# Kernel optimization log

Hardware: AMD Instinct MI355X
Metric: run time of the kernel (lower is better)

Reference implementation:

```python
import jax, jax.numpy as jnp
import numpy as np

B, DIM, L = 4, 1024, 4096
N_CODES, CODE_DIM, H = 512, 256, 8
D = DIM // H  # head_dim = 128


def setup_inputs() -> dict:
    key = jax.random.key(0)
    k1, k2, k3, k4 = jax.random.split(key, 4)
    return {
        "x": jax.random.normal(k1, (B, DIM, L), dtype=jnp.float32),
        "codes": jax.random.normal(k2, (N_CODES, CODE_DIM), dtype=jnp.float32),
        "Wk": jax.random.normal(k3, (CODE_DIM, H, D), dtype=jnp.float32) * (CODE_DIM ** -0.5),
        "Wv": jax.random.normal(k4, (CODE_DIM, H, D), dtype=jnp.float32) * (CODE_DIM ** -0.5),
    }


def reference(x, codes, Wk, Wv):
    b, xdim, l = x.shape
    h, d = Wk.shape[1], Wk.shape[2]
    scale = d ** -0.5
    # b (h d) l -> b h l d
    q = scale * jnp.transpose(x.reshape(b, h, d, l), (0, 1, 3, 2))
    k = jnp.einsum('nc,chd->hnd', codes, Wk)  # [H, N, D]
    v = jnp.einsum('nc,chd->hnd', codes, Wv)  # [H, N, D]
    logits = jnp.einsum('bhld,hmd->bhlm', q, k)  # [B, H, L, N]
    idx = jnp.argmax(logits, axis=-1)  # [B, H, L] int
    # hard one-hot attention == direct gather from v
    h_ix = jnp.arange(h)[None, :, None]  # broadcast over B, L
    out = v[h_ix, idx]  # [B, H, L, D]
    out = jnp.transpose(out, (0, 1, 3, 2)).reshape(b, h * d, l)  # b (h d) l
    return out, idx
```

## Files before the change

kernel.cpp:

```cpp
#include <hip/hip_runtime.h>
#include <cstdint>

#define L_ 4096
#define NC_ 512
#define CD_ 256
#define H_ 8
#define D_ 128
#define B_ 4
#define SCALE 0.08838834764831845f
#define TAU 3.0e-3f

typedef _Float16 f16x8 __attribute__((ext_vector_type(8)));
typedef _Float16 f16x4 __attribute__((ext_vector_type(4)));
typedef float f32x16 __attribute__((ext_vector_type(16)));
typedef float f32x4 __attribute__((ext_vector_type(4)));

__global__ __launch_bounds__(256) void kv_pre(
    const float* __restrict__ codes, const float* __restrict__ Wk,
    const float* __restrict__ Wv, _Float16* __restrict__ K16f,
    float* __restrict__ K32, float* __restrict__ V)
{
    __shared__ float clds[16][260];
    const int t = threadIdx.x, h = blockIdx.y, n0 = blockIdx.x * 16;
    const int dz = blockIdx.z;
    {
        #pragma unroll
        for (int i = 0; i < 4; ++i) {
            int j = t + i*256;
            int row = j >> 6, c4 = j & 63;
            *(float4*)&clds[row][c4*4] =
                *(const float4*)(codes + (size_t)(n0 + row)*CD_ + c4*4);
        }
    }
    __syncthreads();
    const int nl = t >> 4;
    const int dq = t & 15;
    const int d0 = dz*64 + dq*4;
    const int n  = n0 + nl;
    float ak0=0,ak1=0,ak2=0,ak3=0, av0=0,av1=0,av2=0,av3=0;
    const float4* wk4 = (const float4*)Wk;
    const float4* wv4 = (const float4*)Wv;
    for (int c = 0; c < CD_; c += 4) {
        float4 cv = *(const float4*)&clds[nl][c];
        #pragma unroll
        for (int u = 0; u < 4; ++u) {
            float cu = (u==0)?cv.x:(u==1)?cv.y:(u==2)?cv.z:cv.w;
            float4 wk = wk4[((size_t)(c+u)*H_ + h)*32 + (d0>>2)];
            float4 wv = wv4[((size_t)(c+u)*H_ + h)*32 + (d0>>2)];
            ak0 = fmaf(cu, wk.x, ak0); ak1 = fmaf(cu, wk.y, ak1);
            ak2 = fmaf(cu, wk.z, ak2); ak3 = fmaf(cu, wk.w, ak3);
            av0 = fmaf(cu, wv.x, av0); av1 = fmaf(cu, wv.y, av1);
            av2 = fmaf(cu, wv.z, av2); av3 = fmaf(cu, wv.w, av3);
        }
    }
    const size_t r32 = ((size_t)(h*NC_ + n))*D_ + d0;
    float4 sk; sk.x=ak0; sk.y=ak1; sk.z=ak2; sk.w=ak3;
    float4 sv; sv.x=av0; sv.y=av1; sv.z=av2; sv.w=av3;
    *(float4*)(K32 + r32) = sk;
    *(float4*)(V   + r32) = sv;
    f16x4 hk; hk[0]=(_Float16)ak0; hk[1]=(_Float16)ak1; hk[2]=(_Float16)ak2; hk[3]=(_Float16)ak3;
    const size_t a16 = ((size_t)((h*16 + (n>>5))*8 + (d0>>4))*64
                        + ((n&31) + ((d0>>3)&1)*32))*8 + (d0&7);
    *(f16x4*)(K16f + a16) = hk;
}

#define GLD_LDS16(GP, LP)                                                      \
  __builtin_amdgcn_global_load_lds(                                            \
      (const __attribute__((address_space(1))) void*)(GP),                     \
      (__attribute__((address_space(3))) void*)(LP), 16, 0, 0)

#define WAIT_VM0    asm volatile("s_waitcnt vmcnt(0)" ::: "memory")
#define WAIT_LGKM   asm volatile("s_waitcnt lgkmcnt(0)" ::: "memory")

#define QSTAGE(RD, QS)                                                         \
  _Pragma("unroll")                                                            \
  for (int i_ = 0; i_ < 4; ++i_) {                                             \
    const float* sp_ = xb + (size_t)((RD)*32 + i_*8 + (lane>>3))*L_            \
                          + l0w + (lane&7)*4;                                  \
    GLD_LDS16(sp_, (char*)(QS) + i_*1024);                                     \
  }

#define QREAD(RD, QS)                                                          \
  _Pragma("unroll")                                                            \
  for (int p_ = 0; p_ < 2; ++p_) {                                             \
    f16x8 tmp_;                                                                \
    _Pragma("unroll")                                                          \
    for (int j_ = 0; j_ < 8; ++j_)                                             \
      tmp_[j_] = (_Float16)(SCALE * (QS)[(p_*16 + hi*8 + j_)*32 + colL]);      \
    qf[(RD)*2 + p_] = tmp_;                                                    \
  }

#define KSTAGE(TI, DST)                                                        \
  GLD_LDS16(kh + ((size_t)(TI)*4096 + (wid*64 + lane)*8),                      \
            (DST) + (size_t)(wid*64)*8);                                       \
  GLD_LDS16(kh + ((size_t)(TI)*4096 + (256 + wid*64 + lane)*8),                \
            (DST) + (size_t)(256 + wid*64)*8);

__global__ __launch_bounds__(256, 4) void attn_main(
    const float* __restrict__ x, const _Float16* __restrict__ K16f,
    const float* __restrict__ K32, const float* __restrict__ V,
    float* __restrict__ out, float* __restrict__ idxf)
{
    __shared__ __align__(16) char smem[32768 + 2048];
    _Float16* bufA = (_Float16*)smem;
    _Float16* bufB = (_Float16*)(smem + 16384);
    float*    qbuf = (float*)(smem + 32768);

    const int t = threadIdx.x;
    const int wid = t >> 6, lane = t & 63;
    const int bid = blockIdx.x;
    const int h  = bid & 7;
    const int rr_ = bid >> 3;
    const int lx = rr_ & 31, b = rr_ >> 5;
    const int l0w = lx * 128 + wid * 32;

    const float* xb = x + ((size_t)(b*1024 + h*128)) * L_;
    const int colL = lane & 31;
    const int hi = lane >> 5;
    const int laneN4 = hi * 4;

    float* qs0 = (float*)(smem + wid * 8192);
    float* qs1 = (float*)(smem + wid * 8192 + 4096);
    f16x8 qf[8];
    QSTAGE(0, qs0)
    QSTAGE(1, qs1)
    WAIT_VM0;
    QREAD(0, qs0)
    QREAD(1, qs1)
    WAIT_LGKM;
    QSTAGE(2, qs0)
    QSTAGE(3, qs1)
    WAIT_VM0;
    QREAD(2, qs0)
    QREAD(3, qs1)
    __syncthreads();

    const _Float16* kh = K16f + ((size_t)h << 16);

    KSTAGE(0, bufA)
    KSTAGE(1, bufA + 4096)

    float v1 = -INFINITY, v2 = -INFINITY, v3 = -INFINITY;
    int i1 = 0, i2 = 0;

    __syncthreads();

    for (int m = 0; m < 8; ++m) {
        _Float16* cur = (m & 1) ? bufB : bufA;
        _Float16* nxt = (m & 1) ? bufA : bufB;
        if (m < 7) {
            KSTAGE(2*m + 2, nxt)
            KSTAGE(2*m + 3, nxt + 4096)
        }
        #pragma unroll
        for (int sub = 0; sub < 2; ++sub) {
            const _Float16* kt = cur + sub*4096;
            f32x16 acc;
            #pragma unroll
            for (int r = 0; r < 16; ++r) acc[r] = 0.f;
            #pragma unroll
            for (int ds = 0; ds < 8; ++ds) {
                f16x8 kf = *(const f16x8*)(kt + (size_t)(ds*64 + lane)*8);
                acc = __builtin_amdgcn_mfma_f32_32x32x16_f16(kf, qf[ds], acc, 0, 0, 0);
            }
            const int nb = (2*m + sub)*32 + laneN4;
            #pragma unroll
            for (int r = 0; r < 16; ++r) {
                const int n = nb + (r & 3) + ((r >> 2) << 3);
                float v = acc[r];
                bool gt1 = v > v1;
                bool gt2 = v > v2;
                i2 = gt1 ? i1 : (gt2 ? n : i2);
                i1 = gt1 ? n  : i1;
                v3 = fmaxf(v3, fminf(v2, v));
                v2 = fmaxf(v2, fminf(v1, v));
                v1 = fmaxf(v1, v);
            }
        }
        __syncthreads();
    }

    float ov1 = __shfl_xor(v1, 32), ov2 = __shfl_xor(v2, 32), ov3 = __shfl_xor(v3, 32);
    int oi1 = __shfl_xor(i1, 32), oi2 = __shfl_xor(i2, 32);
    bool sw = (ov1 > v1) || (ov1 == v1 && oi1 < i1);
    float a1 = sw ? ov1 : v1;  int ai1 = sw ? oi1 : i1;
    float b1 = sw ? v1 : ov1;  int bi1 = sw ? i1 : oi1;
    float a2 = sw ? ov2 : v2;  int ai2 = sw ? oi2 : i2;
    float b2 = sw ? v2 : ov2;
    float a3 = sw ? ov3 : v3;
    bool sec = (b1 > a2) || (b1 == a2 && bi1 < ai2);
    const float V1 = a1;             const int I1 = ai1;
    const float V2 = sec ? b1 : a2;  const int I2 = sec ? bi1 : ai2;
    const float V3 = sec ? fmaxf(a2, b2) : fmaxf(a3, b1);
    int idx = I1;

    const bool cheap = (V1 - V2 < TAU) && (V1 - V3 >= TAU);
    const bool full  = (V1 - V3 < TAU);

    unsigned long long mc = __ballot(cheap) & 0xffffffffull;
    while (mc) {
        int src = (int)__builtin_ctzll(mc); mc &= mc - 1;
        int rl = l0w + src;
        int ra = __shfl(I1, src);
        int rb = __shfl(I2, src);
        int n = hi ? rb : ra;
        f32x4 kk = *(const f32x4*)(K32 + ((size_t)(h*NC_ + n))*D_ + colL*4);
        int dd = colL * 4;
        float q0 = SCALE * xb[(size_t)(dd+0)*L_ + rl];
        float q1 = SCALE * xb[(size_t)(dd+1)*L_ + rl];
        float q2 = SCALE * xb[(size_t)(dd+2)*L_ + rl];
        float q3 = SCALE * xb[(size_t)(dd+3)*L_ + rl];
        float p = q0 * kk[0];
        p = fmaf(q1, kk[1], p); p = fmaf(q2, kk[2], p); p = fmaf(q3, kk[3], p);
        #pragma unroll
        for (int m2 = 1; m2 < 32; m2 <<= 1) p += __shfl_xor(p, m2);
        float va = __shfl(p, 0);
        float vb = __shfl(p, 32);
        bool takeB = (vb > va) || (vb == va && rb < ra);
        int win = takeB ? rb : ra;
        if (lane == src) idx = win;
    }

    unsigned long long mf2 = __ballot(full) & 0xffffffffull;
    float* qb = qbuf + wid * 128;
    while (mf2) {
        int src = (int)__builtin_ctzll(mf2); mf2 &= mf2 - 1;
        int rl = l0w + src;
        qb[lane]      = SCALE * xb[(size_t)lane*L_ + rl];
        qb[lane + 64] = SCALE * xb[(size_t)(lane+64)*L_ + rl];
        __builtin_amdgcn_wave_barrier();
        WAIT_LGKM;
        float q0 = qb[colL*4+0], q1 = qb[colL*4+1], q2 = qb[colL*4+2], q3 = qb[colL*4+3];
        const f32x4* krow = (const f32x4*)(K32 + (size_t)h*NC_*D_);
        float bv = -INFINITY; int bn = 0;
        for (int i = 0; i < 256; i += 4) {
            #pragma unroll
            for (int u = 0; u < 4; ++u) {
                f32x4 kk = krow[(size_t)(i+u)*64 + lane];
                float p = q0 * kk[0];
                p = fmaf(q1, kk[1], p); p = fmaf(q2, kk[2], p); p = fmaf(q3, kk[3], p);
                #pragma unroll
                for (int m2 = 1; m2 < 32; m2 <<= 1) p += __shfl_xor(p, m2);
                const int n = 2*(i+u) + hi;
                if (p > bv) { bv = p; bn = n; }
            }
        }
        {
            float ov = __shfl_xor(bv, 32);
            int on = __shfl_xor(bn, 32);
            if (ov > bv || (ov == bv && on < bn)) { bv = ov; bn = on; }
        }
        if (lane == src) idx = bn;
        __builtin_amdgcn_wave_barrier();
    }
    idx = __shfl(idx, colL);

    const int myl = l0w + colL;
    if (!hi) idxf[((size_t)(b*H_ + h))*L_ + myl] = (float)idx;
    const f32x4* vrow = (const f32x4*)(V + ((size_t)(h*NC_ + idx))*D_);
    float* ob = out + ((size_t)(b*1024 + h*128 + hi*64))*L_ + myl;
    #pragma unroll
    for (int p = 0; p < 16; ++p) {
        f32x4 vv = vrow[hi*16 + p];
        ob[(size_t)(p*4+0)*L_] = vv[0];
        ob[(size_t)(p*4+1)*L_] = vv[1];
        ob[(size_t)(p*4+2)*L_] = vv[2];
        ob[(size_t)(p*4+3)*L_] = vv[3];
    }
}

extern "C" void kernel_launch(void* const* d_in, const int* in_sizes, int n_in,
                              void* d_out, int out_size, void* d_ws, size_t ws_size,
                              hipStream_t stream)
{
    const float* x     = (const float*)d_in[0];
    const float* codes = (const float*)d_in[1];
    const float* Wk    = (const float*)d_in[2];
    const float* Wv    = (const float*)d_in[3];

    float* out  = (float*)d_out;
    float* idxf = out + (size_t)B_ * H_ * D_ * L_;

    _Float16* K16f = (_Float16*)d_ws;
    float*    K32  = (float*)((char*)d_ws + (1u << 20));
    float*    Vf   = (float*)((char*)d_ws + (3u << 20));

    kv_pre<<<dim3(32, 8, 2), 256, 0, stream>>>(codes, Wk, Wv, K16f, K32, Vf);
    attn_main<<<dim3(1024), 256, 0, stream>>>(x, K16f, K32, Vf, out, idxf);
}
```

Baseline: 104.4 us.

## Pack code index into float low bits for branchless top-3 argmax tracking

```diff
diff --git a/kernel.cpp b/kernel.cpp
--- a/kernel.cpp
+++ b/kernel.cpp
@@ -8,7 +8,7 @@
 #define D_ 128
 #define B_ 4
 #define SCALE 0.08838834764831845f
-#define TAU 3.0e-3f
+#define TAU 4.0e-3f
 
 typedef _Float16 f16x8 __attribute__((ext_vector_type(8)));
 typedef _Float16 f16x4 __attribute__((ext_vector_type(4)));
@@ -58,7 +58,9 @@
     float4 sv; sv.x=av0; sv.y=av1; sv.z=av2; sv.w=av3;
     *(float4*)(K32 + r32) = sk;
     *(float4*)(V   + r32) = sv;
-    f16x4 hk; hk[0]=(_Float16)ak0; hk[1]=(_Float16)ak1; hk[2]=(_Float16)ak2; hk[3]=(_Float16)ak3;
+    f16x4 hk;
+    hk[0]=(_Float16)(SCALE*ak0); hk[1]=(_Float16)(SCALE*ak1);
+    hk[2]=(_Float16)(SCALE*ak2); hk[3]=(_Float16)(SCALE*ak3);
     const size_t a16 = ((size_t)((h*16 + (n>>5))*8 + (d0>>4))*64
                         + ((n&31) + ((d0>>3)&1)*32))*8 + (d0&7);
     *(f16x4*)(K16f + a16) = hk;
@@ -86,7 +88,7 @@
     f16x8 tmp_;                                                                \
     _Pragma("unroll")                                                          \
     for (int j_ = 0; j_ < 8; ++j_)                                             \
-      tmp_[j_] = (_Float16)(SCALE * (QS)[(p_*16 + hi*8 + j_)*32 + colL]);      \
+      tmp_[j_] = (_Float16)((QS)[(p_*16 + hi*8 + j_)*32 + colL]);              \
     qf[(RD)*2 + p_] = tmp_;                                                    \
   }
 
@@ -140,8 +142,10 @@
     KSTAGE(0, bufA)
     KSTAGE(1, bufA + 4096)
 
+    int nOr[16];
+    #pragma unroll
+    for (int r = 0; r < 16; ++r) nOr[r] = (r & 3) + ((r >> 2) << 3) + laneN4;
     float v1 = -INFINITY, v2 = -INFINITY, v3 = -INFINITY;
-    int i1 = 0, i2 = 0;
 
     __syncthreads();
 
@@ -163,35 +167,30 @@
                 f16x8 kf = *(const f16x8*)(kt + (size_t)(ds*64 + lane)*8);
                 acc = __builtin_amdgcn_mfma_f32_32x32x16_f16(kf, qf[ds], acc, 0, 0, 0);
             }
-            const int nb = (2*m + sub)*32 + laneN4;
+            const int tb = (2*m + sub)*32;
             #pragma unroll
             for (int r = 0; r < 16; ++r) {
-                const int n = nb + (r & 3) + ((r >> 2) << 3);
-                float v = acc[r];
-                bool gt1 = v > v1;
-                bool gt2 = v > v2;
-                i2 = gt1 ? i1 : (gt2 ? n : i2);
-                i1 = gt1 ? n  : i1;
-                v3 = fmaxf(v3, fminf(v2, v));
-                v2 = fmaxf(v2, fminf(v1, v));
-                v1 = fmaxf(v1, v);
+                int ki = (__float_as_int(acc[r]) & 0xFFFFFE00) | (tb + nOr[r]);
+                float k = __int_as_float(ki);
+                v3 = fmaxf(v3, fminf(fminf(v1, v2), k));
+                float nv2 = __builtin_amdgcn_fmed3f(v1, v2, k);
+                v1 = fmaxf(v1, k);
+                v2 = nv2;
             }
         }
         __syncthreads();
     }
 
-    float ov1 = __shfl_xor(v1, 32), ov2 = __shfl_xor(v2, 32), ov3 = __shfl_xor(v3, 32);
-    int oi1 = __shfl_xor(i1, 32), oi2 = __shfl_xor(i2, 32);
-    bool sw = (ov1 > v1) || (ov1 == v1 && oi1 < i1);
-    float a1 = sw ? ov1 : v1;  int ai1 = sw ? oi1 : i1;
-    float b1 = sw ? v1 : ov1;  int bi1 = sw ? i1 : oi1;
-    float a2 = sw ? ov2 : v2;  int ai2 = sw ? oi2 : i2;
-    float b2 = sw ? v2 : ov2;
-    float a3 = sw ? ov3 : v3;
-    bool sec = (b1 > a2) || (b1 == a2 && bi1 < ai2);
-    const float V1 = a1;             const int I1 = ai1;
-    const float V2 = sec ? b1 : a2;  const int I2 = sec ? bi1 : ai2;
-    const float V3 = sec ? fmaxf(a2, b2) : fmaxf(a3, b1);
+    float b1k = __shfl_xor(v1, 32);
+    float b2k = __shfl_xor(v2, 32);
+    float b3k = __shfl_xor(v3, 32);
+    const float V1 = fmaxf(v1, b1k);
+    const float c1 = fminf(v1, b1k);
+    const float d1 = fmaxf(v2, b2k);
+    const float V2 = fmaxf(c1, d1);
+    const float V3 = __builtin_amdgcn_fmed3f(c1, d1, fmaxf(v3, b3k));
+    const int I1 = __float_as_int(V1) & 511;
+    const int I2 = __float_as_int(V2) & 511;
     int idx = I1;
 
     const bool cheap = (V1 - V2 < TAU) && (V1 - V3 >= TAU);
```

Result: faster. 101.2 us (-3.1%).
